# Kernel optimization log

Hardware: AMD Instinct MI355X
Metric: run time of the kernel (lower is better)

Reference implementation:

```python
import jax, jax.numpy as jnp
import numpy as np

NUM_HEADS = 12


def _quantize_feat(feat, embed):
    # feat: [B,H,M,d], embed: [H,K,d] -> nearest codebook vector per token
    # squared euclidean distance (same argmin as cdist p=2)
    f2 = jnp.sum(feat * feat, axis=-1, keepdims=True)            # [B,H,M,1]
    e2 = jnp.sum(embed * embed, axis=-1)[None, :, None, :]       # [1,H,1,K]
    fe = jnp.einsum('bhmd,hkd->bhmk', feat, embed)               # [B,H,M,K]
    dist = f2 - 2.0 * fe + e2
    idx = jnp.argmin(dist, axis=-1)                              # [B,H,M]
    quant = jnp.take_along_axis(embed[None], idx[..., None], axis=2)  # [B,H,M,d]
    return quant


def setup_inputs() -> dict:
    key = jax.random.key(0)
    ks = jax.random.split(key, 6)
    B, N, C, H, K = 64, 197, 768, NUM_HEADS, 50
    d = C // H
    return {
        'x': jax.random.normal(ks[0], (B, N, C), jnp.float32),
        'qkv_w': jax.random.normal(ks[1], (3 * C, C), jnp.float32) * (C ** -0.5),
        'proj_w': jax.random.normal(ks[2], (C, C), jnp.float32) * (C ** -0.5),
        'proj_b': jnp.zeros((C,), jnp.float32),
        'q_embed': jax.random.normal(ks[3], (H, K, d), jnp.float32),
        'k_embed': jax.random.normal(ks[4], (H, K, d), jnp.float32),
    }


def reference(x, qkv_w, proj_w, proj_b, q_embed, k_embed):
    B, N, C = x.shape
    H = NUM_HEADS
    d = C // H
    scale = d ** -0.5

    qkv = jnp.einsum('bnc,oc->bno', x, qkv_w).reshape(B, N, 3, H, d)
    qkv = jnp.transpose(qkv, (2, 0, 3, 1, 4))                    # [3,B,H,N,d]
    q, k, v = qkv[0], qkv[1], qkv[2]

    attn = jax.nn.softmax(jnp.einsum('bhnd,bhmd->bhnm', q, k) * scale, axis=-1)

    # quantize all tokens except cls (index 0); cls passes through detached
    q_cls = jax.lax.stop_gradient(q[:, :, 0:1, :])
    k_cls = jax.lax.stop_gradient(k[:, :, 0:1, :])
    quant_q = _quantize_feat(q[:, :, 1:, :], q_embed)
    quant_k = _quantize_feat(k[:, :, 1:, :], k_embed)

    cat_q = jnp.concatenate((q_cls, quant_q), axis=2)
    cat_k = jnp.concatenate((k_cls, quant_k), axis=2)
    quant_attn = jax.nn.softmax(
        jnp.einsum('bhnd,bhmd->bhnm', cat_q, cat_k) * scale, axis=-1)

    # losses (matching F.mse_loss mean reduction and F.kl_div semantics,
    # where input is treated as log-probabilities)
    q_tgt = jax.lax.stop_gradient(q[:, :, 1:, :])
    k_tgt = jax.lax.stop_gradient(k[:, :, 1:, :])
    quant_loss = jnp.mean((quant_q - q_tgt) ** 2) + jnp.mean((quant_k - k_tgt) ** 2)
    attn_det = jax.lax.stop_gradient(attn)
    kl = jnp.mean(attn_det * (jnp.log(attn_det) - quant_attn))
    quant_loss = quant_loss + kl

    out = jnp.einsum('bhnm,bhmd->bhnd', quant_attn, v)           # [B,H,N,d]
    out = jnp.transpose(out, (0, 2, 1, 3)).reshape(B, N, C)
    out = jnp.einsum('bnc,oc->bno', out, proj_w) + proj_b
    return (out, quant_loss)
```

## Files before the change

kernel.cpp:

```cpp
#include <hip/hip_runtime.h>
#include <math.h>

#define NB 64
#define NN 197
#define NC 768
#define NH 12
#define ND 64
#define KCB 50
#define NM (NN-1)
#define BNROWS (NB*NN)
#define SZ ((size_t)NB*NH*NN*ND)
#define WQKV ((size_t)2304*768)
#define WPRJ ((size_t)768*768)

typedef unsigned short u16;
typedef unsigned int u32;
typedef unsigned long long u64;
typedef _Float16 h2 __attribute__((ext_vector_type(2)));
typedef _Float16 f16x4 __attribute__((ext_vector_type(4)));
typedef _Float16 f16x8 __attribute__((ext_vector_type(8)));
typedef float f32x4 __attribute__((ext_vector_type(4)));

#define GLOAD16(gp, lp) __builtin_amdgcn_global_load_lds( \
    (const __attribute__((address_space(1))) void*)(gp),  \
    (__attribute__((address_space(3))) void*)(lp), 16, 0, 0)

__device__ __forceinline__ u16 f2h(float x) {
  _Float16 h = (_Float16)x;
  return *(u16*)&h;
}
__device__ __forceinline__ u32 packh2(float a, float b) {
  h2 v = { (_Float16)a, (_Float16)b };
  return *(u32*)&v;
}

template<bool LO>
__global__ __launch_bounds__(256)
void split_kernel(const float* __restrict__ src, u16* __restrict__ hi,
                  u16* __restrict__ lo, int n4)
{
  int i = blockIdx.x*256 + threadIdx.x;
  if (i >= n4) return;
  float4 v = ((const float4*)src)[i];
  _Float16 h0 = (_Float16)v.x, h1 = (_Float16)v.y, h2_ = (_Float16)v.z, h3 = (_Float16)v.w;
  uint2 hv = make_uint2((u32)*(u16*)&h0 | ((u32)*(u16*)&h1 << 16),
                        (u32)*(u16*)&h2_ | ((u32)*(u16*)&h3 << 16));
  ((uint2*)hi)[i] = hv;
  if constexpr (LO) {
    _Float16 l0 = (_Float16)(v.x - (float)h0), l1 = (_Float16)(v.y - (float)h1);
    _Float16 l2 = (_Float16)(v.z - (float)h2_), l3 = (_Float16)(v.w - (float)h3);
    uint2 lv = make_uint2((u32)*(u16*)&l0 | ((u32)*(u16*)&l1 << 16),
                          (u32)*(u16*)&l2 | ((u32)*(u16*)&l3 << 16));
    ((uint2*)lo)[i] = lv;
  }
}

template<int MODE>
__global__ __launch_bounds__(256)
void gemm_mfma(const u16* __restrict__ Ah, const u16* __restrict__ Al,
               const u16* __restrict__ Wh, const u16* __restrict__ Wl,
               float* __restrict__ qb_, float* __restrict__ kb_, u16* __restrict__ vb_,
               const float* __restrict__ bias, float* __restrict__ dout)
{
  constexpr int NPL = (MODE == 1) ? 2 : 4;
  constexpr int NBX = (MODE == 1) ? 6 : 18;
  constexpr int NWG = NBX * 99;
  constexpr int Q8 = NWG / 8, R8 = NWG % 8;
  __shared__ u16 lds[2][NPL][4096];
  const int tid = threadIdx.x;
  const int lane = tid & 63, w = tid >> 6;
  const int wm = w >> 1, wn = w & 1;
  const int wg = blockIdx.x;
  const int xcd = wg & 7, cidx = wg >> 3;
  const int work = (xcd < R8 ? xcd*(Q8+1) : R8*(Q8+1) + (xcd-R8)*Q8) + cidx;
  const int row0 = (work / NBX) * 128, col0 = (work % NBX) * 128;
  const bool dolo = (MODE == 0) && (col0 < 1536);

  f32x4 acc[4][4];
  #pragma unroll
  for (int mi = 0; mi < 4; ++mi)
    #pragma unroll
    for (int ni = 0; ni < 4; ++ni) acc[mi][ni] = (f32x4){0.f, 0.f, 0.f, 0.f};

  auto stage = [&](int buf, int kt) {
    const int c0 = kt * 32;
    #pragma unroll
    for (int j = 0; j < 2; ++j) {
      const int r0 = w*32 + j*16;
      const int lrow = r0 + (lane >> 2);
      const int slot = (lane & 3) ^ (lrow & 3);
      int ar = row0 + lrow; if (ar > BNROWS-1) ar = BNROWS-1;
      const size_t ga = (size_t)ar * 768 + c0 + slot*8;
      const size_t gb = (size_t)(col0 + lrow) * 768 + c0 + slot*8;
      GLOAD16(Ah + ga, &lds[buf][0][r0*32]);
      GLOAD16(Wh + gb, &lds[buf][1][r0*32]);
      if constexpr (MODE == 0) {
        if (dolo) {
          GLOAD16(Al + ga, &lds[buf][2][r0*32]);
          GLOAD16(Wl + gb, &lds[buf][3][r0*32]);
        }
      }
    }
  };

  auto compute = [&](int buf) {
    f16x8 ah[4], bh[4];
    const int g = lane >> 4;
    int offa[4], offb[4];
    #pragma unroll
    for (int mi = 0; mi < 4; ++mi) {
      int arow = wm*64 + mi*16 + (lane & 15);
      offa[mi] = arow*32 + ((g ^ (arow & 3)) << 3);
      ah[mi] = *(const f16x8*)&lds[buf][0][offa[mi]];
    }
    #pragma unroll
    for (int ni = 0; ni < 4; ++ni) {
      int brow = wn*64 + ni*16 + (lane & 15);
      offb[ni] = brow*32 + ((g ^ (brow & 3)) << 3);
      bh[ni] = *(const f16x8*)&lds[buf][1][offb[ni]];
    }
    #pragma unroll
    for (int mi = 0; mi < 4; ++mi)
      #pragma unroll
      for (int ni = 0; ni < 4; ++ni)
        acc[mi][ni] = __builtin_amdgcn_mfma_f32_16x16x32_f16(ah[mi], bh[ni], acc[mi][ni], 0, 0, 0);
    if constexpr (MODE == 0) {
      if (dolo) {
        f16x8 al[4], bl[4];
        #pragma unroll
        for (int mi = 0; mi < 4; ++mi) al[mi] = *(const f16x8*)&lds[buf][2][offa[mi]];
        #pragma unroll
        for (int ni = 0; ni < 4; ++ni) bl[ni] = *(const f16x8*)&lds[buf][3][offb[ni]];
        #pragma unroll
        for (int mi = 0; mi < 4; ++mi)
          #pragma unroll
          for (int ni = 0; ni < 4; ++ni) {
            acc[mi][ni] = __builtin_amdgcn_mfma_f32_16x16x32_f16(ah[mi], bl[ni], acc[mi][ni], 0, 0, 0);
            acc[mi][ni] = __builtin_amdgcn_mfma_f32_16x16x32_f16(al[mi], bh[ni], acc[mi][ni], 0, 0, 0);
          }
      }
    }
  };

  stage(0, 0);
  asm volatile("s_waitcnt vmcnt(0)" ::: "memory");
  __syncthreads();
  int cur = 0;
  for (int kt = 0; kt < 24; ++kt) {
    if (kt < 23) stage(cur ^ 1, kt + 1);
    compute(cur);
    asm volatile("s_waitcnt vmcnt(0)" ::: "memory");
    __syncthreads();
    cur ^= 1;
  }

  float* biasl = nullptr;
  if constexpr (MODE == 1) {
    biasl = (float*)&lds[0][0][0];
    if (tid < 128) biasl[tid] = bias[col0 + tid];
    __syncthreads();
  }
  #pragma unroll
  for (int mi = 0; mi < 4; ++mi) {
    #pragma unroll
    for (int t = 0; t < 4; ++t) {
      int r = row0 + wm*64 + mi*16 + (lane >> 4)*4 + t;
      if (r >= BNROWS) continue;
      if constexpr (MODE == 0) {
        int b_ = r / 197, n_ = r - b_*197;
        #pragma unroll
        for (int ni = 0; ni < 4; ++ni) {
          int o = col0 + wn*64 + ni*16 + (lane & 15);
          float val = acc[mi][ni][t];
          int tq = o / 768, rem = o - tq*768;
          int hh = rem >> 6, dd = rem & 63;
          size_t dst = ((size_t)(b_*12 + hh)*197 + n_)*64 + dd;
          if (tq == 0)      qb_[dst] = val;
          else if (tq == 1) kb_[dst] = val;
          else              vb_[dst] = f2h(val);
        }
      } else {
        #pragma unroll
        for (int ni = 0; ni < 4; ++ni) {
          int o = col0 + wn*64 + ni*16 + (lane & 15);
          dout[(size_t)r*768 + o] = acc[mi][ni][t] + biasl[o - col0];
        }
      }
    }
  }
}

__global__ __launch_bounds__(256)
void quant_mfma(const float* __restrict__ x, const float* __restrict__ qkv_w,
                const float* __restrict__ qbuf, const float* __restrict__ kbuf,
                const float* __restrict__ qe, const float* __restrict__ ke,
                u16* __restrict__ cq, u16* __restrict__ ck, float* __restrict__ pq)
{
  __shared__ __align__(16) float El[KCB*66];
  __shared__ __align__(16) u16 Ehi[64*64];
  __shared__ __align__(16) u16 Elo[64*64];
  __shared__ double e2d[KCB];
  __shared__ int idxb[NM];
  __shared__ float wred[4];
  const int tid = threadIdx.x;
  const int bh = blockIdx.x;
  const int which = blockIdx.y;
  const int b_ = bh / 12, h_ = bh - b_*12;
  const float* feat = which ? kbuf : qbuf;
  const float* emb  = which ? ke : qe;
  u16* dst = which ? ck : cq;
  const size_t base = (size_t)bh * (197*64);
  const int lane = tid & 63, w = tid >> 6;
  const int ln = lane & 15, g = lane >> 4;

  for (int idx = tid; idx < KCB*64; idx += 256) {
    int kk = idx >> 6, i = idx & 63;
    float v = emb[h_*(KCB*64) + idx];
    El[kk*66 + i] = v;
    _Float16 hv = (_Float16)v;
    Ehi[idx] = *(u16*)&hv;
    _Float16 lv = (_Float16)(v - (float)hv);
    Elo[idx] = *(u16*)&lv;
  }
  for (int idx = tid; idx < 14*64; idx += 256) {
    Ehi[KCB*64 + idx] = 0; Elo[KCB*64 + idx] = 0;
  }
  if (tid >= 64 && tid < 128) {
    int i = tid - 64;
    dst[base + i] = f2h(feat[base + i]);
  }
  __syncthreads();
  if (tid < KCB) {
    double s = 0.0;
    for (int i = 0; i < 64; ++i) { double e = (double)El[tid*66 + i]; s += e*e; }
    e2d[tid] = s;
  }
  __syncthreads();

  f16x8 Eah[4][2], Eal[4][2];
  float e2l[4][4];
  #pragma unroll
  for (int t = 0; t < 4; ++t) {
    #pragma unroll
    for (int s = 0; s < 2; ++s) {
      int off = (t*16 + ln)*64 + s*32 + g*8;
      Eah[t][s] = *(const f16x8*)&Ehi[off];
      Eal[t][s] = *(const f16x8*)&Elo[off];
    }
    #pragma unroll
    for (int r = 0; r < 4; ++r) {
      int c = t*16 + g*4 + r;
      e2l[t][r] = (c < KCB) ? (float)e2d[c] : 1e30f;
    }
  }

  float msum = 0.f;
  for (int nt = w; nt < 13; nt += 4) {
    int tok = nt*16 + ln;
    int tokc = tok < NM ? tok : NM-1;
    const float* frow = feat + base + (size_t)(tokc+1)*64;
    f16x8 fqh[2], fql[2];
    float f2 = 0.f;
    #pragma unroll
    for (int s = 0; s < 2; ++s) {
      float4 q0 = *(const float4*)(frow + s*32 + g*8);
      float4 q1 = *(const float4*)(frow + s*32 + g*8 + 4);
      float vv[8] = {q0.x,q0.y,q0.z,q0.w,q1.x,q1.y,q1.z,q1.w};
      f16x8 hv, lv;
      #pragma unroll
      for (int i = 0; i < 8; ++i) {
        _Float16 h = (_Float16)vv[i];
        hv[i] = h;
        lv[i] = (_Float16)(vv[i] - (float)h);
        f2 = fmaf(vv[i], vv[i], f2);
      }
      fqh[s] = hv; fql[s] = lv;
    }
    f32x4 dacc[4];
    #pragma unroll
    for (int t = 0; t < 4; ++t) dacc[t] = (f32x4){0.f,0.f,0.f,0.f};
    #pragma unroll
    for (int t = 0; t < 4; ++t)
      #pragma unroll
      for (int s = 0; s < 2; ++s) {
        dacc[t] = __builtin_amdgcn_mfma_f32_16x16x32_f16(Eah[t][s], fqh[s], dacc[t], 0, 0, 0);
        dacc[t] = __builtin_amdgcn_mfma_f32_16x16x32_f16(Eah[t][s], fql[s], dacc[t], 0, 0, 0);
        dacc[t] = __builtin_amdgcn_mfma_f32_16x16x32_f16(Eal[t][s], fqh[s], dacc[t], 0, 0, 0);
      }
    float d1 = 1e38f, d2 = 1e38f; int idx = 0;
    #pragma unroll
    for (int t = 0; t < 4; ++t)
      #pragma unroll
      for (int r = 0; r < 4; ++r) {
        int c = t*16 + g*4 + r;
        float d = fmaf(-2.f, dacc[t][r], e2l[t][r]);
        if (d < d1) { d2 = d1; d1 = d; idx = c; }
        else if (d < d2) d2 = d;
      }
    #pragma unroll
    for (int off = 16; off <= 32; off <<= 1) {
      float od1 = __shfl_xor(d1, off), od2 = __shfl_xor(d2, off);
      int   oi  = __shfl_xor(idx, off);
      float of2 = __shfl_xor(f2, off);
      f2 += of2;
      if (od1 < d1 || (od1 == d1 && oi < idx)) {
        d2 = fminf(d1, od2); d1 = od1; idx = oi;
      } else {
        d2 = fminf(d2, od1);
      }
    }
    bool valid = tok < NM;
    bool exact = false;
    u64 flags = __ballot(g == 0 && valid && (d2 - d1) < 1e-3f);
    while (flags) {
      int src = __ffsll(flags) - 1;
      flags &= flags - 1;
      int mrow = 1 + nt*16 + src;
      const float* xrow = x + (size_t)(b_*197 + mrow)*768;
      const float* wrow = qkv_w + (size_t)(which*768 + h_*64 + lane)*768;
      double qd0 = 0.0, qd1 = 0.0, qd2 = 0.0, qd3 = 0.0;
      for (int c = 0; c < 768; c += 4) {
        qd0 = fma((double)xrow[c],   (double)wrow[c],   qd0);
        qd1 = fma((double)xrow[c+1], (double)wrow[c+1], qd1);
        qd2 = fma((double)xrow[c+2], (double)wrow[c+2], qd2);
        qd3 = fma((double)xrow[c+3], (double)wrow[c+3], qd3);
      }
      double qd = (qd0 + qd1) + (qd2 + qd3);
      double bb = 1e300; int bi = 0;
      for (int kk = 0; kk < KCB; ++kk) {
        double df = qd - (double)El[kk*66 + lane];
        double sq = df*df;
        #pragma unroll
        for (int off = 32; off > 0; off >>= 1) sq += __shfl_xor(sq, off);
        if (sq < bb) { bb = sq; bi = kk; }
      }
      if (ln == src) { idx = bi; d1 = (float)bb; exact = true; }
    }
    if (g == 0 && valid) {
      idxb[tok] = idx;
      msum += exact ? d1 : (d1 + f2);
    }
  }
  __syncthreads();

  for (int idx = tid; idx < NM*64; idx += 256) {
    int mm = idx >> 6, i = idx & 63;
    dst[base + (size_t)(mm+1)*64 + i] = f2h(El[idxb[mm]*66 + i]);
  }

  #pragma unroll
  for (int off = 8; off > 0; off >>= 1) msum += __shfl_down(msum, off);
  if (lane == 0) wred[w] = msum;
  __syncthreads();
  if (tid == 0) pq[which*768 + bh] = wred[0]+wred[1]+wred[2]+wred[3];
}

__global__ __launch_bounds__(256)
void fused_attn_mfma(const float* __restrict__ qbuf, const float* __restrict__ kbuf,
                     const u16* __restrict__ cq, const u16* __restrict__ ck,
                     const u16* __restrict__ vb,
                     u16* __restrict__ aoh, float* __restrict__ pkl)
{
  __shared__ __align__(16) u16 Kf[200*64];
  __shared__ __align__(16) u16 CKf[200*64];
  __shared__ __align__(16) u16 Vt[64*212];
  __shared__ float wred[4];
  const int tid = threadIdx.x;
  const int bh = blockIdx.x;
  const int b_ = bh / 12, h_ = bh - b_*12;
  const size_t base = (size_t)bh * (197*64);
  const u32* ck32 = (const u32*)ck;
  const u32* vb32 = (const u32*)vb;
  const size_t base2 = base >> 1;

  for (int idx = tid; idx < 197*32; idx += 256) {
    int m = idx >> 5, j = idx & 31;
    int dsti = m*32 + (((j >> 2) ^ (m & 7)) << 2) + (j & 3);
    float2 kv = *(const float2*)(kbuf + base + 2*idx);
    ((u32*)Kf)[dsti] = packh2(kv.x, kv.y);
    ((u32*)CKf)[dsti] = ck32[base2 + idx];
    u32 v2 = vb32[base2 + idx];
    Vt[(2*j)*212 + m]   = (u16)(v2 & 0xffff);
    Vt[(2*j+1)*212 + m] = (u16)(v2 >> 16);
  }
  for (int idx = tid; idx < 96; idx += 256) {
    int m = 197 + (idx >> 5), j = idx & 31;
    int dsti = m*32 + (((j >> 2) ^ (m & 7)) << 2) + (j & 3);
    ((u32*)Kf)[dsti] = 0; ((u32*)CKf)[dsti] = 0;
  }
  for (int idx = tid; idx < 64*15; idx += 256) {
    int d = idx / 15, mc = 197 + idx % 15;
    Vt[d*212 + mc] = 0;
  }
  __syncthreads();

  const int lane = tid & 63, w = tid >> 6;
  const int ln = lane & 15, g = lane >> 4;
  float klacc = 0.f;

  for (int nt = w; nt < 13; nt += 4) {
    const int n0 = nt*16;
    const int nb = n0 + ln;
    const float* qrow = qbuf + base + (size_t)nb*64;
    f16x8 fq[2], fcq[2];
    #pragma unroll
    for (int s = 0; s < 2; ++s) {
      float4 q0 = *(const float4*)(qrow + s*32 + g*8);
      float4 q1 = *(const float4*)(qrow + s*32 + g*8 + 4);
      fq[s] = (f16x8){(_Float16)q0.x,(_Float16)q0.y,(_Float16)q0.z,(_Float16)q0.w,
                      (_Float16)q1.x,(_Float16)q1.y,(_Float16)q1.z,(_Float16)q1.w};
      uint4 cu = *(const uint4*)(cq + base + (size_t)nb*64 + s*32 + g*8);
      *(uint4*)&fcq[s] = cu;
    }

    float Ma = -3e38f, Mq = -3e38f;
    float aS = 0.f, aT = 0.f, qS = 0.f, cross = 0.f;
    f32x4 ov[4];
    #pragma unroll
    for (int dt = 0; dt < 4; ++dt) ov[dt] = (f32x4){0.f,0.f,0.f,0.f};

    for (int t = 0; t < 13; ++t) {
      int mrow = t*16 + ln; if (mrow > 199) mrow = 199;
      const char* kb8 = (const char*)Kf + mrow*128;
      const char* cb8 = (const char*)CKf + mrow*128;
      int sw = (mrow & 7) << 4;
      f32x4 sa = (f32x4){0.f,0.f,0.f,0.f}, sq = (f32x4){0.f,0.f,0.f,0.f};
      sa = __builtin_amdgcn_mfma_f32_16x16x32_f16(*(const f16x8*)(kb8 + (( g     <<4) ^ sw)), fq[0], sa, 0,0,0);
      sa = __builtin_amdgcn_mfma_f32_16x16x32_f16(*(const f16x8*)(kb8 + (((4+g)<<4) ^ sw)), fq[1], sa, 0,0,0);
      sq = __builtin_amdgcn_mfma_f32_16x16x32_f16(*(const f16x8*)(cb8 + (( g     <<4) ^ sw)), fcq[0], sq, 0,0,0);
      sq = __builtin_amdgcn_mfma_f32_16x16x32_f16(*(const f16x8*)(cb8 + (((4+g)<<4) ^ sw)), fcq[1], sq, 0,0,0);
      int mbase = t*16 + g*4;
      float tma = -3e38f, tmq = -3e38f;
      #pragma unroll
      for (int r = 0; r < 4; ++r) {
        bool v = (mbase + r) < 197;
        tma = fmaxf(tma, v ? sa[r] : -3e38f);
        tmq = fmaxf(tmq, v ? sq[r] : -3e38f);
      }
      tma = fmaxf(tma, __shfl_xor(tma, 16)); tma = fmaxf(tma, __shfl_xor(tma, 32));
      tmq = fmaxf(tmq, __shfl_xor(tmq, 16)); tmq = fmaxf(tmq, __shfl_xor(tmq, 32));
      float Ma2 = fmaxf(Ma, tma), Mq2 = fmaxf(Mq, tmq);
      float sca = __expf(0.125f*(Ma - Ma2));
      float scq = __expf(0.125f*(Mq - Mq2));
      Ma = Ma2; Mq = Mq2;
      aS *= sca; aT *= sca; qS *= scq; cross *= sca*scq;
      float s0 = __shfl(scq, g*4+0), s1 = __shfl(scq, g*4+1);
      float s2 = __shfl(scq, g*4+2), s3 = __shfl(scq, g*4+3);
      #pragma unroll
      for (int dt = 0; dt < 4; ++dt) {
        ov[dt][0] *= s0; ov[dt][1] *= s1; ov[dt][2] *= s2; ov[dt][3] *= s3;
      }
      const float mla = 0.125f*Ma, mlq = 0.125f*Mq;
      float eqv[4];
      #pragma unroll
      for (int r = 0; r < 4; ++r) {
        bool v = (mbase + r) < 197;
        float ea = v ? __expf(fmaf(sa[r], 0.125f, -mla)) : 0.f;
        float eq = v ? __expf(fmaf(sq[r], 0.125f, -mlq)) : 0.f;
        aS += ea;
        aT = fmaf(ea, sa[r], aT);
        qS += eq;
        cross = fmaf(ea, eq, cross);
        eqv[r] = eq;
      }
      f16x4 qaf = {(_Float16)eqv[0], (_Float16)eqv[1], (_Float16)eqv[2], (_Float16)eqv[3]};
      #pragma unroll
      for (int dt = 0; dt < 4; ++dt) {
        f16x4 bv = *(const f16x4*)(Vt + (dt*16 + ln)*212 + t*16 + g*4);
        ov[dt] = __builtin_amdgcn_mfma_f32_16x16x16f16(qaf, bv, ov[dt], 0, 0, 0);
      }
    }
    aS += __shfl_xor(aS, 16); aS += __shfl_xor(aS, 32);
    aT += __shfl_xor(aT, 16); aT += __shfl_xor(aT, 32);
    qS += __shfl_xor(qS, 16); qS += __shfl_xor(qS, 32);
    cross += __shfl_xor(cross, 16); cross += __shfl_xor(cross, 32);

    if (g == 0 && nb < 197) {
      float rowkl = 0.125f*(aT/aS) - 0.125f*Ma - __logf(aS) - cross/(aS*qS);
      klacc += rowkl;
    }
    #pragma unroll
    for (int r = 0; r < 4; ++r) {
      int nl = g*4 + r;
      int nglob = n0 + nl;
      if (nglob >= 197) continue;
      float qSn = __shfl(qS, nl);
      float inv = __frcp_rn(qSn);
      size_t obase = ((size_t)(b_*197 + nglob))*768 + h_*64;
      #pragma unroll
      for (int dt = 0; dt < 4; ++dt)
        aoh[obase + dt*16 + ln] = f2h(ov[dt][r] * inv);
    }
  }

  #pragma unroll
  for (int off = 32; off > 0; off >>= 1) klacc += __shfl_down(klacc, off);
  if (lane == 0) wred[w] = klacc;
  __syncthreads();
  if (tid == 0) pkl[bh] = wred[0] + wred[1] + wred[2] + wred[3];
}

__global__ __launch_bounds__(256)
void finalize_kernel(const float* __restrict__ pq, const float* __restrict__ pkl,
                     float* __restrict__ dout)
{
  __shared__ double red[256];
  const int tid = threadIdx.x;
  double s0 = 0.0, s1 = 0.0;
  for (int i = tid; i < 1536; i += 256) s0 += (double)pq[i];
  for (int i = tid; i < 768; i += 256) s1 += (double)pkl[i];
  red[tid] = s0; __syncthreads();
  for (int off = 128; off > 0; off >>= 1) { if (tid < off) red[tid] += red[tid+off]; __syncthreads(); }
  double mse = red[0];
  __syncthreads();
  red[tid] = s1; __syncthreads();
  for (int off = 128; off > 0; off >>= 1) { if (tid < off) red[tid] += red[tid+off]; __syncthreads(); }
  double kl = red[0];
  if (tid == 0) dout[SZ] = (float)(mse / 9633792.0 + kl / 29805312.0);
}

extern "C" void kernel_launch(void* const* d_in, const int* in_sizes, int n_in,
                              void* d_out, int out_size, void* d_ws, size_t ws_size,
                              hipStream_t stream)
{
  const float* x      = (const float*)d_in[0];
  const float* qkv_w  = (const float*)d_in[1];
  const float* proj_w = (const float*)d_in[2];
  const float* proj_b = (const float*)d_in[3];
  const float* qe     = (const float*)d_in[4];
  const float* ke     = (const float*)d_in[5];
  float* out = (float*)d_out;

  float* ws  = (float*)d_ws;
  float* qb_ = ws;
  float* kb_ = ws + SZ;
  u16*   vb_ = (u16*)(ws + 2*SZ);
  u16*   cq_ = vb_ + SZ;
  u16*   ck_ = cq_ + SZ;
  u16*   xh_ = ck_ + SZ;
  u16*   xl_ = xh_ + SZ;
  u16*   aoh_= xl_ + SZ;
  u16*   wh_ = aoh_ + SZ;
  u16*   wl_ = wh_ + WQKV;
  u16*   ph_ = wl_ + WQKV;
  float* pq_ = (float*)(ph_ + WPRJ);
  float* pkl_= pq_ + 1536;

  dim3 blk(256);
  split_kernel<true><<<dim3((int)(SZ/4/256)),   blk, 0, stream>>>(x, xh_, xl_, (int)(SZ/4));
  split_kernel<true><<<dim3((int)(WQKV/4/256)), blk, 0, stream>>>(qkv_w, wh_, wl_, (int)(WQKV/4));
  split_kernel<false><<<dim3((int)(WPRJ/4/256)), blk, 0, stream>>>(proj_w, ph_, nullptr, (int)(WPRJ/4));
  gemm_mfma<0><<<dim3(99*18), blk, 0, stream>>>(xh_, xl_, wh_, wl_, qb_, kb_, vb_, nullptr, nullptr);
  quant_mfma<<<dim3(768, 2), blk, 0, stream>>>(x, qkv_w, qb_, kb_, qe, ke, cq_, ck_, pq_);
  fused_attn_mfma<<<dim3(768), blk, 0, stream>>>(qb_, kb_, cq_, ck_, vb_, aoh_, pkl_);
  gemm_mfma<1><<<dim3(99*6), blk, 0, stream>>>(aoh_, nullptr, ph_, nullptr, nullptr, nullptr, nullptr, proj_b, out);
  finalize_kernel<<<dim3(1), blk, 0, stream>>>(pq_, pkl_, out);
}
```

Baseline: 351.2 us.

## Fuse x fp16 split into QKV GEMM and store q/k as fp16 hi/lo pairs

Drops the separate split kernel for x. The QKV GEMM now loads fp32 x tiles straight into LDS and splits them into fp16 hi/lo in registers. The GEMM epilogue writes q and k as fp16 hi and lo halves instead of fp32, so the quant and attention kernels read half-precision pairs and skip their own conversions. This removes one full pass over x and halves the q/k intermediate traffic. In exchange, A-tile LDS use doubles and the GEMM inner loop does extra conversion work.

```diff
diff --git a/kernel.cpp b/kernel.cpp
--- a/kernel.cpp
+++ b/kernel.cpp
@@ -29,10 +29,7 @@
   _Float16 h = (_Float16)x;
   return *(u16*)&h;
 }
-__device__ __forceinline__ u32 packh2(float a, float b) {
-  h2 v = { (_Float16)a, (_Float16)b };
-  return *(u32*)&v;
-}
+__device__ __forceinline__ float h2f(u16 b) { _Float16 h = *(_Float16*)&b; return (float)h; }
 
 template<bool LO>
 __global__ __launch_bounds__(256)
@@ -57,16 +54,17 @@
 
 template<int MODE>
 __global__ __launch_bounds__(256)
-void gemm_mfma(const u16* __restrict__ Ah, const u16* __restrict__ Al,
+void gemm_mfma(const float* __restrict__ Af, const u16* __restrict__ Ah,
                const u16* __restrict__ Wh, const u16* __restrict__ Wl,
-               float* __restrict__ qb_, float* __restrict__ kb_, u16* __restrict__ vb_,
+               u16* __restrict__ qh_, u16* __restrict__ ql_,
+               u16* __restrict__ kh_, u16* __restrict__ kl_, u16* __restrict__ vb_,
                const float* __restrict__ bias, float* __restrict__ dout)
 {
-  constexpr int NPL = (MODE == 1) ? 2 : 4;
+  constexpr int BUF = (MODE == 0) ? 32768 : 16384;
   constexpr int NBX = (MODE == 1) ? 6 : 18;
   constexpr int NWG = NBX * 99;
   constexpr int Q8 = NWG / 8, R8 = NWG % 8;
-  __shared__ u16 lds[2][NPL][4096];
+  __shared__ __align__(16) char smem[2*BUF];
   const int tid = threadIdx.x;
   const int lane = tid & 63, w = tid >> 6;
   const int wm = w >> 1, wn = w & 1;
@@ -84,53 +82,74 @@
 
   auto stage = [&](int buf, int kt) {
     const int c0 = kt * 32;
-    #pragma unroll
-    for (int j = 0; j < 2; ++j) {
-      const int r0 = w*32 + j*16;
-      const int lrow = r0 + (lane >> 2);
-      const int slot = (lane & 3) ^ (lrow & 3);
-      int ar = row0 + lrow; if (ar > BNROWS-1) ar = BNROWS-1;
-      const size_t ga = (size_t)ar * 768 + c0 + slot*8;
-      const size_t gb = (size_t)(col0 + lrow) * 768 + c0 + slot*8;
-      GLOAD16(Ah + ga, &lds[buf][0][r0*32]);
-      GLOAD16(Wh + gb, &lds[buf][1][r0*32]);
-      if constexpr (MODE == 0) {
-        if (dolo) {
-          GLOAD16(Al + ga, &lds[buf][2][r0*32]);
-          GLOAD16(Wl + gb, &lds[buf][3][r0*32]);
+    char* sb = smem + buf*BUF;
+    if constexpr (MODE == 0) {
+      #pragma unroll
+      for (int j = 0; j < 4; ++j) {
+        int lrow = w*32 + j*8 + (lane >> 3);
+        int slot = (lane & 7) ^ (lrow & 7);
+        int ar = row0 + lrow; if (ar > BNROWS-1) ar = BNROWS-1;
+        GLOAD16(Af + (size_t)ar*768 + c0 + slot*4, sb + (size_t)(w*32 + j*8)*128);
+      }
+      #pragma unroll
+      for (int j = 0; j < 2; ++j) {
+        int lrow = w*32 + j*16 + (lane >> 2);
+        int slot = (lane & 3) ^ (lrow & 3);
+        size_t gb = (size_t)(col0 + lrow)*768 + c0 + slot*8;
+        GLOAD16(Wh + gb, sb + 16384 + (size_t)(w*32 + j*16)*64);
+        if (dolo) GLOAD16(Wl + gb, sb + 24576 + (size_t)(w*32 + j*16)*64);
+      }
+    } else {
+      #pragma unroll
+      for (int j = 0; j < 2; ++j) {
+        int lrow = w*32 + j*16 + (lane >> 2);
+        int slot = (lane & 3) ^ (lrow & 3);
+        int ar = row0 + lrow; if (ar > BNROWS-1) ar = BNROWS-1;
+        GLOAD16(Ah + (size_t)ar*768 + c0 + slot*8, sb + (size_t)(w*32 + j*16)*64);
+        GLOAD16(Wh + (size_t)(col0 + lrow)*768 + c0 + slot*8,
+                sb + 8192 + (size_t)(w*32 + j*16)*64);
+      }
+    }
+  };
+
+  auto compute = [&](int buf) {
+    f16x8 ah[4], al[4], bh[4], bl[4];
+    const int g = lane >> 4;
+    char* sb = smem + buf*BUF;
+    if constexpr (MODE == 0) {
+      const float* Afl = (const float*)sb;
+      #pragma unroll
+      for (int mi = 0; mi < 4; ++mi) {
+        int arow = wm*64 + mi*16 + (lane & 15);
+        float4 a0 = *(const float4*)(Afl + arow*32 + (((2*g)   ^ (arow & 7)) << 2));
+        float4 a1 = *(const float4*)(Afl + arow*32 + (((2*g+1) ^ (arow & 7)) << 2));
+        float av[8] = {a0.x,a0.y,a0.z,a0.w,a1.x,a1.y,a1.z,a1.w};
+        f16x8 hv, lv;
+        #pragma unroll
+        for (int i = 0; i < 8; ++i) {
+          _Float16 h = (_Float16)av[i];
+          hv[i] = h;
+          lv[i] = (_Float16)(av[i] - (float)h);
         }
-      }
-    }
-  };
-
-  auto compute = [&](int buf) {
-    f16x8 ah[4], bh[4];
-    const int g = lane >> 4;
-    int offa[4], offb[4];
-    #pragma unroll
-    for (int mi = 0; mi < 4; ++mi) {
-      int arow = wm*64 + mi*16 + (lane & 15);
-      offa[mi] = arow*32 + ((g ^ (arow & 3)) << 3);
-      ah[mi] = *(const f16x8*)&lds[buf][0][offa[mi]];
-    }
-    #pragma unroll
-    for (int ni = 0; ni < 4; ++ni) {
-      int brow = wn*64 + ni*16 + (lane & 15);
-      offb[ni] = brow*32 + ((g ^ (brow & 3)) << 3);
-      bh[ni] = *(const f16x8*)&lds[buf][1][offb[ni]];
-    }
-    #pragma unroll
-    for (int mi = 0; mi < 4; ++mi)
-      #pragma unroll
-      for (int ni = 0; ni < 4; ++ni)
-        acc[mi][ni] = __builtin_amdgcn_mfma_f32_16x16x32_f16(ah[mi], bh[ni], acc[mi][ni], 0, 0, 0);
-    if constexpr (MODE == 0) {
+        ah[mi] = hv; al[mi] = lv;
+      }
+      const u16* Whl = (const u16*)(sb + 16384);
+      const u16* Wll = (const u16*)(sb + 24576);
+      int offb[4];
+      #pragma unroll
+      for (int ni = 0; ni < 4; ++ni) {
+        int brow = wn*64 + ni*16 + (lane & 15);
+        offb[ni] = brow*32 + ((g ^ (brow & 3)) << 3);
+        bh[ni] = *(const f16x8*)&Whl[offb[ni]];
+      }
+      #pragma unroll
+      for (int mi = 0; mi < 4; ++mi)
+        #pragma unroll
+        for (int ni = 0; ni < 4; ++ni)
+          acc[mi][ni] = __builtin_amdgcn_mfma_f32_16x16x32_f16(ah[mi], bh[ni], acc[mi][ni], 0, 0, 0);
       if (dolo) {
-        f16x8 al[4], bl[4];
-        #pragma unroll
-        for (int mi = 0; mi < 4; ++mi) al[mi] = *(const f16x8*)&lds[buf][2][offa[mi]];
-        #pragma unroll
-        for (int ni = 0; ni < 4; ++ni) bl[ni] = *(const f16x8*)&lds[buf][3][offb[ni]];
+        #pragma unroll
+        for (int ni = 0; ni < 4; ++ni) bl[ni] = *(const f16x8*)&Wll[offb[ni]];
         #pragma unroll
         for (int mi = 0; mi < 4; ++mi)
           #pragma unroll
@@ -139,6 +158,24 @@
             acc[mi][ni] = __builtin_amdgcn_mfma_f32_16x16x32_f16(al[mi], bh[ni], acc[mi][ni], 0, 0, 0);
           }
       }
+    } else {
+      const u16* Ahl = (const u16*)sb;
+      const u16* Whl = (const u16*)(sb + 8192);
+      #pragma unroll
+      for (int mi = 0; mi < 4; ++mi) {
+        int arow = wm*64 + mi*16 + (lane & 15);
+        ah[mi] = *(const f16x8*)&Ahl[arow*32 + ((g ^ (arow & 3)) << 3)];
+      }
+      #pragma unroll
+      for (int ni = 0; ni < 4; ++ni) {
+        int brow = wn*64 + ni*16 + (lane & 15);
+        bh[ni] = *(const f16x8*)&Whl[brow*32 + ((g ^ (brow & 3)) << 3)];
+      }
+      #pragma unroll
+      for (int mi = 0; mi < 4; ++mi)
+        #pragma unroll
+        for (int ni = 0; ni < 4; ++ni)
+          acc[mi][ni] = __builtin_amdgcn_mfma_f32_16x16x32_f16(ah[mi], bh[ni], acc[mi][ni], 0, 0, 0);
     }
   };
 
@@ -156,7 +193,7 @@
 
   float* biasl = nullptr;
   if constexpr (MODE == 1) {
-    biasl = (float*)&lds[0][0][0];
+    biasl = (float*)smem;
     if (tid < 128) biasl[tid] = bias[col0 + tid];
     __syncthreads();
   }
@@ -175,9 +212,10 @@
           int tq = o / 768, rem = o - tq*768;
           int hh = rem >> 6, dd = rem & 63;
           size_t dst = ((size_t)(b_*12 + hh)*197 + n_)*64 + dd;
-          if (tq == 0)      qb_[dst] = val;
-          else if (tq == 1) kb_[dst] = val;
-          else              vb_[dst] = f2h(val);
+          u16 hi = f2h(val);
+          if (tq == 0)      { qh_[dst] = hi; ql_[dst] = f2h(val - h2f(hi)); }
+          else if (tq == 1) { kh_[dst] = hi; kl_[dst] = f2h(val - h2f(hi)); }
+          else              vb_[dst] = hi;
         }
       } else {
         #pragma unroll
@@ -192,7 +230,8 @@
 
 __global__ __launch_bounds__(256)
 void quant_mfma(const float* __restrict__ x, const float* __restrict__ qkv_w,
-                const float* __restrict__ qbuf, const float* __restrict__ kbuf,
+                const u16* __restrict__ qh, const u16* __restrict__ ql,
+                const u16* __restrict__ kh, const u16* __restrict__ kl,
                 const float* __restrict__ qe, const float* __restrict__ ke,
                 u16* __restrict__ cq, u16* __restrict__ ck, float* __restrict__ pq)
 {
@@ -206,7 +245,8 @@
   const int bh = blockIdx.x;
   const int which = blockIdx.y;
   const int b_ = bh / 12, h_ = bh - b_*12;
-  const float* feat = which ? kbuf : qbuf;
+  const u16* feath = which ? kh : qh;
+  const u16* featl = which ? kl : ql;
   const float* emb  = which ? ke : qe;
   u16* dst = which ? ck : cq;
   const size_t base = (size_t)bh * (197*64);
@@ -227,7 +267,7 @@
   }
   if (tid >= 64 && tid < 128) {
     int i = tid - 64;
-    dst[base + i] = f2h(feat[base + i]);
+    dst[base + i] = feath[base + i];
   }
   __syncthreads();
   if (tid < KCB) {
@@ -258,23 +298,21 @@
   for (int nt = w; nt < 13; nt += 4) {
     int tok = nt*16 + ln;
     int tokc = tok < NM ? tok : NM-1;
-    const float* frow = feat + base + (size_t)(tokc+1)*64;
+    const u16* fh = feath + base + (size_t)(tokc+1)*64;
+    const u16* fl = featl + base + (size_t)(tokc+1)*64;
     f16x8 fqh[2], fql[2];
     float f2 = 0.f;
     #pragma unroll
     for (int s = 0; s < 2; ++s) {
-      float4 q0 = *(const float4*)(frow + s*32 + g*8);
-      float4 q1 = *(const float4*)(frow + s*32 + g*8 + 4);
-      float vv[8] = {q0.x,q0.y,q0.z,q0.w,q1.x,q1.y,q1.z,q1.w};
-      f16x8 hv, lv;
+      uint4 uh = *(const uint4*)(fh + s*32 + g*8);
+      uint4 ul = *(const uint4*)(fl + s*32 + g*8);
+      fqh[s] = *(f16x8*)&uh;
+      fql[s] = *(f16x8*)&ul;
       #pragma unroll
       for (int i = 0; i < 8; ++i) {
-        _Float16 h = (_Float16)vv[i];
-        hv[i] = h;
-        lv[i] = (_Float16)(vv[i] - (float)h);
-        f2 = fmaf(vv[i], vv[i], f2);
-      }
-      fqh[s] = hv; fql[s] = lv;
+        float q = (float)fqh[s][i] + (float)fql[s][i];
+        f2 = fmaf(q, q, f2);
+      }
     }
     f32x4 dacc[4];
     #pragma unroll
@@ -356,7 +394,7 @@
 }
 
 __global__ __launch_bounds__(256)
-void fused_attn_mfma(const float* __restrict__ qbuf, const float* __restrict__ kbuf,
+void fused_attn_mfma(const u16* __restrict__ qh, const u16* __restrict__ kh,
                      const u16* __restrict__ cq, const u16* __restrict__ ck,
                      const u16* __restrict__ vb,
                      u16* __restrict__ aoh, float* __restrict__ pkl)
@@ -369,6 +407,7 @@
   const int bh = blockIdx.x;
   const int b_ = bh / 12, h_ = bh - b_*12;
   const size_t base = (size_t)bh * (197*64);
+  const u32* kh32 = (const u32*)kh;
   const u32* ck32 = (const u32*)ck;
   const u32* vb32 = (const u32*)vb;
   const size_t base2 = base >> 1;
@@ -376,8 +415,7 @@
   for (int idx = tid; idx < 197*32; idx += 256) {
     int m = idx >> 5, j = idx & 31;
     int dsti = m*32 + (((j >> 2) ^ (m & 7)) << 2) + (j & 3);
-    float2 kv = *(const float2*)(kbuf + base + 2*idx);
-    ((u32*)Kf)[dsti] = packh2(kv.x, kv.y);
+    ((u32*)Kf)[dsti] = kh32[base2 + idx];
     ((u32*)CKf)[dsti] = ck32[base2 + idx];
     u32 v2 = vb32[base2 + idx];
     Vt[(2*j)*212 + m]   = (u16)(v2 & 0xffff);
@@ -401,16 +439,13 @@
   for (int nt = w; nt < 13; nt += 4) {
     const int n0 = nt*16;
     const int nb = n0 + ln;
-    const float* qrow = qbuf + base + (size_t)nb*64;
     f16x8 fq[2], fcq[2];
     #pragma unroll
     for (int s = 0; s < 2; ++s) {
-      float4 q0 = *(const float4*)(qrow + s*32 + g*8);
-      float4 q1 = *(const float4*)(qrow + s*32 + g*8 + 4);
-      fq[s] = (f16x8){(_Float16)q0.x,(_Float16)q0.y,(_Float16)q0.z,(_Float16)q0.w,
-                      (_Float16)q1.x,(_Float16)q1.y,(_Float16)q1.z,(_Float16)q1.w};
+      uint4 qu = *(const uint4*)(qh + base + (size_t)nb*64 + s*32 + g*8);
+      fq[s] = *(f16x8*)&qu;
       uint4 cu = *(const uint4*)(cq + base + (size_t)nb*64 + s*32 + g*8);
-      *(uint4*)&fcq[s] = cu;
+      fcq[s] = *(f16x8*)&cu;
     }
 
     float Ma = -3e38f, Mq = -3e38f;
@@ -531,28 +566,27 @@
   const float* ke     = (const float*)d_in[5];
   float* out = (float*)d_out;
 
-  float* ws  = (float*)d_ws;
-  float* qb_ = ws;
-  float* kb_ = ws + SZ;
-  u16*   vb_ = (u16*)(ws + 2*SZ);
-  u16*   cq_ = vb_ + SZ;
-  u16*   ck_ = cq_ + SZ;
-  u16*   xh_ = ck_ + SZ;
-  u16*   xl_ = xh_ + SZ;
-  u16*   aoh_= xl_ + SZ;
-  u16*   wh_ = aoh_ + SZ;
-  u16*   wl_ = wh_ + WQKV;
-  u16*   ph_ = wl_ + WQKV;
+  u16* ws16 = (u16*)d_ws;
+  u16* qh_ = ws16;
+  u16* ql_ = qh_ + SZ;
+  u16* kh_ = ql_ + SZ;
+  u16* kl_ = kh_ + SZ;
+  u16* vb_ = kl_ + SZ;
+  u16* cq_ = vb_ + SZ;
+  u16* ck_ = cq_ + SZ;
+  u16* aoh_= ck_ + SZ;
+  u16* wh_ = aoh_ + SZ;
+  u16* wl_ = wh_ + WQKV;
+  u16* ph_ = wl_ + WQKV;
   float* pq_ = (float*)(ph_ + WPRJ);
   float* pkl_= pq_ + 1536;
 
   dim3 blk(256);
-  split_kernel<true><<<dim3((int)(SZ/4/256)),   blk, 0, stream>>>(x, xh_, xl_, (int)(SZ/4));
   split_kernel<true><<<dim3((int)(WQKV/4/256)), blk, 0, stream>>>(qkv_w, wh_, wl_, (int)(WQKV/4));
   split_kernel<false><<<dim3((int)(WPRJ/4/256)), blk, 0, stream>>>(proj_w, ph_, nullptr, (int)(WPRJ/4));
-  gemm_mfma<0><<<dim3(99*18), blk, 0, stream>>>(xh_, xl_, wh_, wl_, qb_, kb_, vb_, nullptr, nullptr);
-  quant_mfma<<<dim3(768, 2), blk, 0, stream>>>(x, qkv_w, qb_, kb_, qe, ke, cq_, ck_, pq_);
-  fused_attn_mfma<<<dim3(768), blk, 0, stream>>>(qb_, kb_, cq_, ck_, vb_, aoh_, pkl_);
-  gemm_mfma<1><<<dim3(99*6), blk, 0, stream>>>(aoh_, nullptr, ph_, nullptr, nullptr, nullptr, nullptr, proj_b, out);
+  gemm_mfma<0><<<dim3(99*18), blk, 0, stream>>>(x, nullptr, wh_, wl_, qh_, ql_, kh_, kl_, vb_, nullptr, nullptr);
+  quant_mfma<<<dim3(768, 2), blk, 0, stream>>>(x, qkv_w, qh_, ql_, kh_, kl_, qe, ke, cq_, ck_, pq_);
+  fused_attn_mfma<<<dim3(768), blk, 0, stream>>>(qh_, kh_, cq_, ck_, vb_, aoh_, pkl_);
+  gemm_mfma<1><<<dim3(99*6), blk, 0, stream>>>(nullptr, aoh_, ph_, nullptr, nullptr, nullptr, nullptr, nullptr, nullptr, proj_b, out);
   finalize_kernel<<<dim3(1), blk, 0, stream>>>(pq_, pkl_, out);
 }
```

Result: no change. 348.5 us (-0.8%).
